# Kernel tuning notes

Measured on AMD Instinct MI355X. Metric: run time of the kernel, lower is better.

## Reference

```python
import jax, jax.numpy as jnp
import numpy as np

B, T, C, H = 2, 2048, 1024, 16
HD = C // H  # head dim = 64


def setup_inputs() -> dict:
    key = jax.random.key(0)
    ks = jax.random.split(key, 5)
    s = 0.02  # GPT-style init scale for weights
    return {
        "x": jax.random.normal(ks[0], (B, T, C), dtype=jnp.float32),
        "Wq": jax.random.normal(ks[1], (C, C), dtype=jnp.float32) * s,
        "bq": jnp.zeros((C,), dtype=jnp.float32),
        "Wk": jax.random.normal(ks[2], (C, C), dtype=jnp.float32) * s,
        "bk": jnp.zeros((C,), dtype=jnp.float32),
        "Wv": jax.random.normal(ks[3], (C, C), dtype=jnp.float32) * s,
        "bv": jnp.zeros((C,), dtype=jnp.float32),
        "Wp": jax.random.normal(ks[4], (C, C), dtype=jnp.float32) * s,
        "bp": jnp.zeros((C,), dtype=jnp.float32),
    }


def reference(x, Wq, bq, Wk, bk, Wv, bv, Wp, bp):
    b, t, c = x.shape
    # torch nn.Linear: y = x @ W.T + b  (W is [out, in])
    def heads(W, bias):
        y = jnp.einsum("btc,oc->bto", x, W) + bias
        return y.reshape(b, t, H, HD).transpose(0, 2, 1, 3)  # [B,H,T,hd]

    q = heads(Wq, bq)
    k = heads(Wk, bk)
    v = heads(Wv, bv)

    scale = 1.0 / np.sqrt(HD).astype(np.float32)
    att = jnp.einsum("bhqd,bhkd->bhqk", q, k) * scale  # [B,H,T,T]
    causal = jnp.tril(jnp.ones((t, t), dtype=bool))
    att = jnp.where(causal[None, None], att, -jnp.inf)
    att = jax.nn.softmax(att, axis=-1)
    # attn_pdrop = 0.0 -> dropout is identity
    y = jnp.einsum("bhqk,bhkd->bhqd", att, v)  # [B,H,T,hd]
    y = y.transpose(0, 2, 1, 3).reshape(b, t, c)
    y = jnp.einsum("btc,oc->bto", y, Wp) + bp  # resid_pdrop = 0.0
    return y
```

## Files before the change

### kernel.cpp

```cpp
#include <hip/hip_runtime.h>
#include <hip/hip_bf16.h>

using bf16 = __hip_bfloat16;
typedef __attribute__((ext_vector_type(8))) short short8;
typedef __attribute__((ext_vector_type(4))) float floatx4;

#define B_  2
#define T_  2048
#define C_  1024
#define H_  16
#define HD_ 64
#define BT_ (B_*T_)
#define NX_ ((size_t)BT_*C_)
#define NW_ ((size_t)C_*C_)
#define PSTR 136
#define KSCQ 0.1803368801f

__device__ __forceinline__ void gl2lds16(const bf16* g, bf16* l) {
    __builtin_amdgcn_global_load_lds((const __attribute__((address_space(1))) unsigned int*)g,
                                     (__attribute__((address_space(3))) unsigned int*)l,
                                     16, 0, 0);
}

__global__ __launch_bounds__(256) void cvt_f32_bf16(
    const float* __restrict__ x,
    const float* __restrict__ Wq, const float* __restrict__ Wk,
    const float* __restrict__ Wv, const float* __restrict__ Wp,
    bf16* __restrict__ xb, bf16* __restrict__ wqb, bf16* __restrict__ wkb,
    bf16* __restrict__ wvb, bf16* __restrict__ wpb)
{
    size_t i4 = ((size_t)blockIdx.x * 256 + threadIdx.x) * 4;
    const float* src; bf16* dst; size_t off;
    if (i4 < NX_) { src = x; dst = xb; off = i4; }
    else {
        size_t j = i4 - NX_;
        int r = (int)(j >> 20);
        off = j & (NW_ - 1);
        src = (r==0) ? Wq : (r==1) ? Wk : (r==2) ? Wv : Wp;
        dst = (r==0) ? wqb : (r==1) ? wkb : (r==2) ? wvb : wpb;
    }
    float4 v = *(const float4*)(src + off);
    union { bf16 h[4]; uint2 u; } o;
    o.h[0] = __float2bfloat16(v.x); o.h[1] = __float2bfloat16(v.y);
    o.h[2] = __float2bfloat16(v.z); o.h[3] = __float2bfloat16(v.w);
    *(uint2*)(dst + off) = o.u;
}

__global__ __launch_bounds__(256) void qkv_gemm(
    const bf16* __restrict__ x,
    const bf16* __restrict__ Wq, const float* __restrict__ bq,
    const bf16* __restrict__ Wk, const float* __restrict__ bk,
    const bf16* __restrict__ Wv, const float* __restrict__ bv,
    bf16* __restrict__ qo, bf16* __restrict__ ko, bf16* __restrict__ vt)
{
    __shared__ __align__(16) bf16 As[128*32];
    __shared__ __align__(16) bf16 Bs[128*32];

    const int tid  = threadIdx.x;
    const int w    = tid >> 6, lane = tid & 63;
    const int g    = lane >> 4, c16 = lane & 15;
    const int wr   = w >> 1,    wc  = w & 1;
    const int mtile = blockIdx.x, ntile = blockIdx.y;
    const int wsel  = ntile >> 3;
    const bf16*  W    = (wsel==0) ? Wq : (wsel==1 ? Wk : Wv);
    const float* bias = (wsel==0) ? bq : (wsel==1 ? bk : bv);
    const float oscale = (wsel==0) ? KSCQ : 1.0f;
    const int nbase  = (ntile & 7) * 128;

    const bf16* ag = x + (size_t)(mtile*128)*C_;
    const bf16* bg = W + (size_t)nbase*C_;

    floatx4 acc[4][4] = {};

    for (int k0 = 0; k0 < C_; k0 += 32) {
        #pragma unroll
        for (int p = 0; p < 2; ++p) {
            int cb = p*256 + w*64;
            int c  = cb + lane;
            gl2lds16(ag + (size_t)(c>>2)*C_ + k0 + (c&3)*8, As + cb*8);
            gl2lds16(bg + (size_t)(c>>2)*C_ + k0 + (c&3)*8, Bs + cb*8);
        }
        __syncthreads();

        short8 af[4], bfr[4];
        #pragma unroll
        for (int i = 0; i < 4; ++i)
            af[i] = *(const short8*)(As + (wr*64 + i*16 + c16)*32 + g*8);
        #pragma unroll
        for (int j = 0; j < 4; ++j)
            bfr[j] = *(const short8*)(Bs + (wc*64 + j*16 + c16)*32 + g*8);
        #pragma unroll
        for (int i = 0; i < 4; ++i)
            #pragma unroll
            for (int j = 0; j < 4; ++j)
                acc[i][j] = __builtin_amdgcn_mfma_f32_16x16x32_bf16(af[i], bfr[j], acc[i][j], 0, 0, 0);
        __syncthreads();
    }

    #pragma unroll
    for (int i = 0; i < 4; ++i) {
        int m0 = mtile*128 + wr*64 + i*16 + g*4;
        #pragma unroll
        for (int j = 0; j < 4; ++j) {
            int n = nbase + wc*64 + j*16 + c16;
            float bvf = bias[n];
            if (wsel == 2) {
                int bb = m0 >> 11, t0 = m0 & (T_-1);
                int hh = n >> 6,  hd = n & 63;
                union { bf16 hv[4]; uint2 u; } tmp;
                #pragma unroll
                for (int r = 0; r < 4; ++r) tmp.hv[r] = __float2bfloat16(acc[i][j][r] + bvf);
                *(uint2*)(vt + ((size_t)((bb*H_ + hh)*64 + hd))*T_ + t0) = tmp.u;
            } else {
                bf16* dst = (wsel==0) ? qo : ko;
                #pragma unroll
                for (int r = 0; r < 4; ++r)
                    dst[(size_t)(m0+r)*C_ + n] = __float2bfloat16((acc[i][j][r] + bvf) * oscale);
            }
        }
    }
}

__global__ __launch_bounds__(128, 2) void attn(
    const bf16* __restrict__ q, const bf16* __restrict__ k,
    const bf16* __restrict__ vt, bf16* __restrict__ y)
{
    __shared__ __align__(16) bf16    Ps[2][2][16*PSTR];
    __shared__ __align__(16) floatx4 MO[2][2][4][64];
    __shared__ __align__(16) floatx4 ML[2][2][64];
    __shared__               float   Mm[2][2][16];

    const int tid = threadIdx.x, w = tid >> 6, lane = tid & 63;
    const int g = lane >> 4, c16 = lane & 15;
    const int blk = blockIdx.x;
    const int p = blk & 31, bh = blk >> 5;
    const int h = bh & 15, b = bh >> 4;

    const bf16* kbase = k  + ((size_t)(b*T_))*C_ + h*64;
    const bf16* vbase = vt + ((size_t)(b*H_ + h))*64*T_;
    const short ONEB = 0x3F80;
    const short8 ones = {ONEB,ONEB,ONEB,ONEB,ONEB,ONEB,ONEB,ONEB};

    #pragma unroll 1
    for (int seg = 0; seg < 2; ++seg) {
        const int j  = seg ? p : 63 - p;
        const int q0 = j * 32;
        const int nit = (j >> 2) + 1;

        short8 aq[2][2];
        #pragma unroll
        for (int rt = 0; rt < 2; ++rt)
            #pragma unroll
            for (int kg = 0; kg < 2; ++kg)
                aq[rt][kg] = *(const short8*)(q + ((size_t)(b*T_ + q0 + rt*16 + c16))*C_
                                                + h*64 + kg*32 + g*8);

        floatx4 accO[2][4] = {};
        floatx4 lacc[2] = {};
        float m_l[2] = {-1e30f, -1e30f};

        #pragma unroll 1
        for (int kt = w; kt < nit; kt += 2) {
            const bf16* kp = kbase + (size_t)(kt*128 + c16)*C_ + g*8;
            short8 kb[8][2];
            #pragma unroll
            for (int ct = 0; ct < 8; ++ct)
                #pragma unroll
                for (int kg = 0; kg < 2; ++kg)
                    kb[ct][kg] = *(const short8*)(kp + (size_t)(ct*16)*C_ + kg*32);
            const bf16* vp = vbase + (size_t)c16*T_ + kt*128 + g*8;
            short8 vb[4][4];
            #pragma unroll
            for (int ks = 0; ks < 4; ++ks)
                #pragma unroll
                for (int nt = 0; nt < 4; ++nt)
                    vb[ks][nt] = *(const short8*)(vp + (size_t)(nt*16)*T_ + ks*32);

            floatx4 s[2][8];
            #pragma unroll
            for (int rt = 0; rt < 2; ++rt)
                #pragma unroll
                for (int ct = 0; ct < 8; ++ct) {
                    floatx4 a = {0.f, 0.f, 0.f, 0.f};
                    a = __builtin_amdgcn_mfma_f32_16x16x32_bf16(kb[ct][0], aq[rt][0], a, 0, 0, 0);
                    a = __builtin_amdgcn_mfma_f32_16x16x32_bf16(kb[ct][1], aq[rt][1], a, 0, 0, 0);
                    s[rt][ct] = a;
                }

            if (kt == nit-1) {
                #pragma unroll
                for (int rt = 0; rt < 2; ++rt) {
                    int qglob = q0 + rt*16 + c16;
                    #pragma unroll
                    for (int ct = 0; ct < 8; ++ct)
                        #pragma unroll
                        for (int r = 0; r < 4; ++r) {
                            int key = kt*128 + ct*16 + g*4 + r;
                            if (key > qglob) s[rt][ct][r] = -1e30f;
                        }
                }
            }

            #pragma unroll
            for (int rt = 0; rt < 2; ++rt) {
                float cm[8];
                #pragma unroll
                for (int ct = 0; ct < 8; ++ct)
                    cm[ct] = fmaxf(fmaxf(s[rt][ct][0], s[rt][ct][1]),
                                   fmaxf(s[rt][ct][2], s[rt][ct][3]));
                float tmax = fmaxf(fmaxf(fmaxf(cm[0], cm[1]), fmaxf(cm[2], cm[3])),
                                   fmaxf(fmaxf(cm[4], cm[5]), fmaxf(cm[6], cm[7])));
                tmax = fmaxf(tmax, __shfl_xor(tmax, 16));
                tmax = fmaxf(tmax, __shfl_xor(tmax, 32));
                float mn = fmaxf(m_l[rt], tmax);
                float alpha = exp2f(m_l[rt] - mn);
                m_l[rt] = mn;

                float ar[4];
                #pragma unroll
                for (int r = 0; r < 4; ++r) ar[r] = __shfl(alpha, g*4 + r);
                #pragma unroll
                for (int r = 0; r < 4; ++r) {
                    lacc[rt][r] *= ar[r];
                    #pragma unroll
                    for (int nt = 0; nt < 4; ++nt) accO[rt][nt][r] *= ar[r];
                }

                #pragma unroll
                for (int ct = 0; ct < 8; ++ct) {
                    float p0 = exp2f(s[rt][ct][0] - mn);
                    float p1 = exp2f(s[rt][ct][1] - mn);
                    float p2 = exp2f(s[rt][ct][2] - mn);
                    float p3 = exp2f(s[rt][ct][3] - mn);
                    union { __hip_bfloat162 h2[2]; uint2 u; } pk;
                    pk.h2[0] = __float22bfloat162_rn(float2{p0, p1});
                    pk.h2[1] = __float22bfloat162_rn(float2{p2, p3});
                    *(uint2*)(Ps[w][rt] + c16*PSTR + ct*16 + g*4) = pk.u;
                }
                short8 pa[4];
                #pragma unroll
                for (int ks = 0; ks < 4; ++ks)
                    pa[ks] = *(const short8*)(Ps[w][rt] + c16*PSTR + ks*32 + g*8);
                #pragma unroll
                for (int ks = 0; ks < 4; ++ks) {
                    lacc[rt] = __builtin_amdgcn_mfma_f32_16x16x32_bf16(pa[ks], ones, lacc[rt], 0, 0, 0);
                    #pragma unroll
                    for (int nt = 0; nt < 4; ++nt)
                        accO[rt][nt] = __builtin_amdgcn_mfma_f32_16x16x32_bf16(pa[ks], vb[ks][nt], accO[rt][nt], 0, 0, 0);
                }
            }
        }

        #pragma unroll
        for (int rt = 0; rt < 2; ++rt) {
            if (g == 0) Mm[w][rt][c16] = m_l[rt];
            ML[w][rt][lane] = lacc[rt];
            #pragma unroll
            for (int nt = 0; nt < 4; ++nt) MO[w][rt][nt][lane] = accO[rt][nt];
        }
        __syncthreads();

        {
            const int rt = w;
            float aA[4], aB[4];
            #pragma unroll
            for (int r = 0; r < 4; ++r) {
                float mA = Mm[0][rt][g*4 + r];
                float mB = Mm[1][rt][g*4 + r];
                float mm = fmaxf(mA, mB);
                aA[r] = exp2f(mA - mm);
                aB[r] = exp2f(mB - mm);
            }
            floatx4 lA = ML[0][rt][lane], lB = ML[1][rt][lane];
            float ir[4];
            #pragma unroll
            for (int r = 0; r < 4; ++r)
                ir[r] = __builtin_amdgcn_rcpf(lA[r]*aA[r] + lB[r]*aB[r]);
            #pragma unroll
            for (int nt = 0; nt < 4; ++nt) {
                floatx4 OA = MO[0][rt][nt][lane], OB = MO[1][rt][nt][lane];
                #pragma unroll
                for (int r = 0; r < 4; ++r) {
                    int row = q0 + rt*16 + g*4 + r;
                    float o = (OA[r]*aA[r] + OB[r]*aB[r]) * ir[r];
                    y[((size_t)(b*T_ + row))*C_ + h*64 + nt*16 + c16] = __float2bfloat16(o);
                }
            }
        }
        __syncthreads();
    }
}

__global__ __launch_bounds__(256) void proj_gemm(
    const bf16* __restrict__ yin, const bf16* __restrict__ Wp, const float* __restrict__ bp,
    float* __restrict__ out)
{
    __shared__ __align__(16) bf16 As[64*32];
    __shared__ __align__(16) bf16 Bs[128*32];

    const int tid = threadIdx.x;
    const int w = tid >> 6, lane = tid & 63;
    const int g = lane >> 4, c16 = lane & 15;
    const int wr = w >> 1, wc = w & 1;
    const int mtile = blockIdx.x, ntile = blockIdx.y;
    const int nbase = ntile * 128;

    const bf16* ag = yin + (size_t)(mtile*64)*C_;
    const bf16* bg = Wp  + (size_t)nbase*C_;

    floatx4 acc[2][4] = {};

    for (int k0 = 0; k0 < C_; k0 += 32) {
        {
            int cb = w*64;
            int c  = cb + lane;
            gl2lds16(ag + (size_t)(c>>2)*C_ + k0 + (c&3)*8, As + cb*8);
        }
        #pragma unroll
        for (int p = 0; p < 2; ++p) {
            int cb = p*256 + w*64;
            int c  = cb + lane;
            gl2lds16(bg + (size_t)(c>>2)*C_ + k0 + (c&3)*8, Bs + cb*8);
        }
        __syncthreads();

        short8 af[2], bfr[4];
        #pragma unroll
        for (int i = 0; i < 2; ++i)
            af[i] = *(const short8*)(As + (wr*32 + i*16 + c16)*32 + g*8);
        #pragma unroll
        for (int j = 0; j < 4; ++j)
            bfr[j] = *(const short8*)(Bs + (wc*64 + j*16 + c16)*32 + g*8);
        #pragma unroll
        for (int i = 0; i < 2; ++i)
            #pragma unroll
            for (int j = 0; j < 4; ++j)
                acc[i][j] = __builtin_amdgcn_mfma_f32_16x16x32_bf16(af[i], bfr[j], acc[i][j], 0, 0, 0);
        __syncthreads();
    }

    #pragma unroll
    for (int i = 0; i < 2; ++i) {
        int m0 = mtile*64 + wr*32 + i*16 + g*4;
        #pragma unroll
        for (int j = 0; j < 4; ++j) {
            int n = nbase + wc*64 + j*16 + c16;
            float bvf = bp[n];
            #pragma unroll
            for (int r = 0; r < 4; ++r)
                out[(size_t)(m0+r)*C_ + n] = acc[i][j][r] + bvf;
        }
    }
}

extern "C" void kernel_launch(void* const* d_in, const int* in_sizes, int n_in,
                              void* d_out, int out_size, void* d_ws, size_t ws_size,
                              hipStream_t stream) {
    const float* x  = (const float*)d_in[0];
    const float* Wq = (const float*)d_in[1];
    const float* bq = (const float*)d_in[2];
    const float* Wk = (const float*)d_in[3];
    const float* bk = (const float*)d_in[4];
    const float* Wv = (const float*)d_in[5];
    const float* bv = (const float*)d_in[6];
    const float* Wp = (const float*)d_in[7];
    const float* bp = (const float*)d_in[8];

    bf16* xb  = (bf16*)d_ws;
    bf16* wqb = xb  + NX_;
    bf16* wkb = wqb + NW_;
    bf16* wvb = wkb + NW_;
    bf16* wpb = wvb + NW_;
    bf16* qw  = wpb + NW_;
    bf16* kw  = qw  + NX_;
    bf16* vt  = kw  + NX_;
    bf16* yw  = vt  + NX_;

    const int cvt_blocks = (int)((NX_ + 4*NW_) / (4*256));
    cvt_f32_bf16<<<cvt_blocks, 256, 0, stream>>>(x, Wq, Wk, Wv, Wp, xb, wqb, wkb, wvb, wpb);
    qkv_gemm<<<dim3(32, 24), 256, 0, stream>>>(xb, wqb, bq, wkb, bk, wvb, bv, qw, kw, vt);
    attn    <<<1024, 128, 0, stream>>>(qw, kw, vt, yw);
    proj_gemm<<<dim3(64, 8), 256, 0, stream>>>(yw, wpb, bp, (float*)d_out);
}
```

Baseline: 217.1 us.

## Share K/V tiles in LDS across four query waves in attention

Restructures the attention kernel so each 256-thread block owns a 128-query tile. Its four waves each take 32 queries and share K and V tiles staged into LDS with global_load_lds. This replaces the old two-wave split over key tiles, which needed an LDS-based softmax merge, and cuts redundant global K/V fragment loads by sharing them across waves. In exchange it adds two block barriers per key tile with no double buffering, and load balance now depends only on reversing the tile order for the second batch instead of pairing short and long segments.

```diff
diff --git a/kernel.cpp b/kernel.cpp
--- a/kernel.cpp
+++ b/kernel.cpp
@@ -121,173 +121,146 @@
     }
 }
 
-__global__ __launch_bounds__(128, 2) void attn(
+__global__ __launch_bounds__(256, 2) void attn(
     const bf16* __restrict__ q, const bf16* __restrict__ k,
     const bf16* __restrict__ vt, bf16* __restrict__ y)
 {
-    __shared__ __align__(16) bf16    Ps[2][2][16*PSTR];
-    __shared__ __align__(16) floatx4 MO[2][2][4][64];
-    __shared__ __align__(16) floatx4 ML[2][2][64];
-    __shared__               float   Mm[2][2][16];
+    __shared__ __align__(16) bf16 Ks[16*512];
+    __shared__ __align__(16) bf16 Vs[16*512];
+    __shared__ __align__(16) bf16 Ps[4][2][16*PSTR];
 
     const int tid = threadIdx.x, w = tid >> 6, lane = tid & 63;
     const int g = lane >> 4, c16 = lane & 15;
-    const int blk = blockIdx.x;
-    const int p = blk & 31, bh = blk >> 5;
-    const int h = bh & 15, b = bh >> 4;
+    const int qraw = blockIdx.x, h = blockIdx.y, b = blockIdx.z;
+    const int qt = b ? 15 - qraw : qraw;
+    const int nit = qt + 1;
+    const int q0 = qt*128 + w*32;
 
     const bf16* kbase = k  + ((size_t)(b*T_))*C_ + h*64;
     const bf16* vbase = vt + ((size_t)(b*H_ + h))*64*T_;
     const short ONEB = 0x3F80;
     const short8 ones = {ONEB,ONEB,ONEB,ONEB,ONEB,ONEB,ONEB,ONEB};
 
+    short8 aq[2][2];
+    #pragma unroll
+    for (int rt = 0; rt < 2; ++rt)
+        #pragma unroll
+        for (int kg = 0; kg < 2; ++kg)
+            aq[rt][kg] = *(const short8*)(q + ((size_t)(b*T_ + q0 + rt*16 + c16))*C_
+                                            + h*64 + kg*32 + g*8);
+
+    floatx4 accO[2][4] = {};
+    floatx4 lacc[2] = {};
+    float m_l[2] = {-1e30f, -1e30f};
+
     #pragma unroll 1
-    for (int seg = 0; seg < 2; ++seg) {
-        const int j  = seg ? p : 63 - p;
-        const int q0 = j * 32;
-        const int nit = (j >> 2) + 1;
-
-        short8 aq[2][2];
-        #pragma unroll
-        for (int rt = 0; rt < 2; ++rt)
-            #pragma unroll
-            for (int kg = 0; kg < 2; ++kg)
-                aq[rt][kg] = *(const short8*)(q + ((size_t)(b*T_ + q0 + rt*16 + c16))*C_
-                                                + h*64 + kg*32 + g*8);
-
-        floatx4 accO[2][4] = {};
-        floatx4 lacc[2] = {};
-        float m_l[2] = {-1e30f, -1e30f};
-
-        #pragma unroll 1
-        for (int kt = w; kt < nit; kt += 2) {
-            const bf16* kp = kbase + (size_t)(kt*128 + c16)*C_ + g*8;
-            short8 kb[8][2];
+    for (int kt = 0; kt < nit; ++kt) {
+        #pragma unroll
+        for (int p = 0; p < 4; ++p) {
+            int f = w*4 + p;
+            int ctk = f >> 1, kg = f & 1;
+            gl2lds16(kbase + (size_t)(kt*128 + ctk*16 + c16)*C_ + kg*32 + g*8, Ks + f*512);
+            gl2lds16(vbase + (size_t)(p*16 + c16)*T_ + kt*128 + w*32 + g*8,    Vs + f*512);
+        }
+        __syncthreads();
+
+        floatx4 s[2][8];
+        #pragma unroll
+        for (int ct = 0; ct < 8; ++ct) {
+            short8 kb0 = *(const short8*)(Ks + (ct*2 + 0)*512 + lane*8);
+            short8 kb1 = *(const short8*)(Ks + (ct*2 + 1)*512 + lane*8);
+            #pragma unroll
+            for (int rt = 0; rt < 2; ++rt) {
+                floatx4 a = {0.f, 0.f, 0.f, 0.f};
+                a = __builtin_amdgcn_mfma_f32_16x16x32_bf16(kb0, aq[rt][0], a, 0, 0, 0);
+                a = __builtin_amdgcn_mfma_f32_16x16x32_bf16(kb1, aq[rt][1], a, 0, 0, 0);
+                s[rt][ct] = a;
+            }
+        }
+
+        if (kt == nit-1) {
+            #pragma unroll
+            for (int rt = 0; rt < 2; ++rt) {
+                int qglob = q0 + rt*16 + c16;
+                #pragma unroll
+                for (int ct = 0; ct < 8; ++ct)
+                    #pragma unroll
+                    for (int r = 0; r < 4; ++r) {
+                        int key = kt*128 + ct*16 + g*4 + r;
+                        if (key > qglob) s[rt][ct][r] = -1e30f;
+                    }
+            }
+        }
+
+        #pragma unroll
+        for (int rt = 0; rt < 2; ++rt) {
+            float cm[8];
             #pragma unroll
             for (int ct = 0; ct < 8; ++ct)
-                #pragma unroll
-                for (int kg = 0; kg < 2; ++kg)
-                    kb[ct][kg] = *(const short8*)(kp + (size_t)(ct*16)*C_ + kg*32);
-            const bf16* vp = vbase + (size_t)c16*T_ + kt*128 + g*8;
-            short8 vb[4][4];
-            #pragma unroll
-            for (int ks = 0; ks < 4; ++ks)
+                cm[ct] = fmaxf(fmaxf(s[rt][ct][0], s[rt][ct][1]),
+                               fmaxf(s[rt][ct][2], s[rt][ct][3]));
+            float tmax = fmaxf(fmaxf(fmaxf(cm[0], cm[1]), fmaxf(cm[2], cm[3])),
+                               fmaxf(fmaxf(cm[4], cm[5]), fmaxf(cm[6], cm[7])));
+            tmax = fmaxf(tmax, __shfl_xor(tmax, 16));
+            tmax = fmaxf(tmax, __shfl_xor(tmax, 32));
+            float mn = fmaxf(m_l[rt], tmax);
+            float alpha = exp2f(m_l[rt] - mn);
+            m_l[rt] = mn;
+
+            float ar[4];
+            #pragma unroll
+            for (int r = 0; r < 4; ++r) ar[r] = __shfl(alpha, g*4 + r);
+            #pragma unroll
+            for (int r = 0; r < 4; ++r) {
+                lacc[rt][r] *= ar[r];
+                #pragma unroll
+                for (int nt = 0; nt < 4; ++nt) accO[rt][nt][r] *= ar[r];
+            }
+
+            #pragma unroll
+            for (int ct = 0; ct < 8; ++ct) {
+                float p0 = exp2f(s[rt][ct][0] - mn);
+                float p1 = exp2f(s[rt][ct][1] - mn);
+                float p2 = exp2f(s[rt][ct][2] - mn);
+                float p3 = exp2f(s[rt][ct][3] - mn);
+                union { __hip_bfloat162 h2[2]; uint2 u; } pk;
+                pk.h2[0] = __float22bfloat162_rn(float2{p0, p1});
+                pk.h2[1] = __float22bfloat162_rn(float2{p2, p3});
+                *(uint2*)(Ps[w][rt] + c16*PSTR + ct*16 + g*4) = pk.u;
+            }
+        }
+
+        #pragma unroll
+        for (int ks = 0; ks < 4; ++ks) {
+            short8 vb[4];
+            #pragma unroll
+            for (int nt = 0; nt < 4; ++nt)
+                vb[nt] = *(const short8*)(Vs + (ks*4 + nt)*512 + lane*8);
+            #pragma unroll
+            for (int rt = 0; rt < 2; ++rt) {
+                short8 pa = *(const short8*)(Ps[w][rt] + c16*PSTR + ks*32 + g*8);
+                lacc[rt] = __builtin_amdgcn_mfma_f32_16x16x32_bf16(pa, ones, lacc[rt], 0, 0, 0);
                 #pragma unroll
                 for (int nt = 0; nt < 4; ++nt)
-                    vb[ks][nt] = *(const short8*)(vp + (size_t)(nt*16)*T_ + ks*32);
-
-            floatx4 s[2][8];
-            #pragma unroll
-            for (int rt = 0; rt < 2; ++rt)
-                #pragma unroll
-                for (int ct = 0; ct < 8; ++ct) {
-                    floatx4 a = {0.f, 0.f, 0.f, 0.f};
-                    a = __builtin_amdgcn_mfma_f32_16x16x32_bf16(kb[ct][0], aq[rt][0], a, 0, 0, 0);
-                    a = __builtin_amdgcn_mfma_f32_16x16x32_bf16(kb[ct][1], aq[rt][1], a, 0, 0, 0);
-                    s[rt][ct] = a;
-                }
-
-            if (kt == nit-1) {
-                #pragma unroll
-                for (int rt = 0; rt < 2; ++rt) {
-                    int qglob = q0 + rt*16 + c16;
-                    #pragma unroll
-                    for (int ct = 0; ct < 8; ++ct)
-                        #pragma unroll
-                        for (int r = 0; r < 4; ++r) {
-                            int key = kt*128 + ct*16 + g*4 + r;
-                            if (key > qglob) s[rt][ct][r] = -1e30f;
-                        }
-                }
-            }
-
-            #pragma unroll
-            for (int rt = 0; rt < 2; ++rt) {
-                float cm[8];
-                #pragma unroll
-                for (int ct = 0; ct < 8; ++ct)
-                    cm[ct] = fmaxf(fmaxf(s[rt][ct][0], s[rt][ct][1]),
-                                   fmaxf(s[rt][ct][2], s[rt][ct][3]));
-                float tmax = fmaxf(fmaxf(fmaxf(cm[0], cm[1]), fmaxf(cm[2], cm[3])),
-                                   fmaxf(fmaxf(cm[4], cm[5]), fmaxf(cm[6], cm[7])));
-                tmax = fmaxf(tmax, __shfl_xor(tmax, 16));
-                tmax = fmaxf(tmax, __shfl_xor(tmax, 32));
-                float mn = fmaxf(m_l[rt], tmax);
-                float alpha = exp2f(m_l[rt] - mn);
-                m_l[rt] = mn;
-
-                float ar[4];
-                #pragma unroll
-                for (int r = 0; r < 4; ++r) ar[r] = __shfl(alpha, g*4 + r);
-                #pragma unroll
-                for (int r = 0; r < 4; ++r) {
-                    lacc[rt][r] *= ar[r];
-                    #pragma unroll
-                    for (int nt = 0; nt < 4; ++nt) accO[rt][nt][r] *= ar[r];
-                }
-
-                #pragma unroll
-                for (int ct = 0; ct < 8; ++ct) {
-                    float p0 = exp2f(s[rt][ct][0] - mn);
-                    float p1 = exp2f(s[rt][ct][1] - mn);
-                    float p2 = exp2f(s[rt][ct][2] - mn);
-                    float p3 = exp2f(s[rt][ct][3] - mn);
-                    union { __hip_bfloat162 h2[2]; uint2 u; } pk;
-                    pk.h2[0] = __float22bfloat162_rn(float2{p0, p1});
-                    pk.h2[1] = __float22bfloat162_rn(float2{p2, p3});
-                    *(uint2*)(Ps[w][rt] + c16*PSTR + ct*16 + g*4) = pk.u;
-                }
-                short8 pa[4];
-                #pragma unroll
-                for (int ks = 0; ks < 4; ++ks)
-                    pa[ks] = *(const short8*)(Ps[w][rt] + c16*PSTR + ks*32 + g*8);
-                #pragma unroll
-                for (int ks = 0; ks < 4; ++ks) {
-                    lacc[rt] = __builtin_amdgcn_mfma_f32_16x16x32_bf16(pa[ks], ones, lacc[rt], 0, 0, 0);
-                    #pragma unroll
-                    for (int nt = 0; nt < 4; ++nt)
-                        accO[rt][nt] = __builtin_amdgcn_mfma_f32_16x16x32_bf16(pa[ks], vb[ks][nt], accO[rt][nt], 0, 0, 0);
-                }
-            }
-        }
-
-        #pragma unroll
-        for (int rt = 0; rt < 2; ++rt) {
-            if (g == 0) Mm[w][rt][c16] = m_l[rt];
-            ML[w][rt][lane] = lacc[rt];
-            #pragma unroll
-            for (int nt = 0; nt < 4; ++nt) MO[w][rt][nt][lane] = accO[rt][nt];
-        }
-        __syncthreads();
-
-        {
-            const int rt = w;
-            float aA[4], aB[4];
+                    accO[rt][nt] = __builtin_amdgcn_mfma_f32_16x16x32_bf16(pa, vb[nt], accO[rt][nt], 0, 0, 0);
+            }
+        }
+        __syncthreads();
+    }
+
+    #pragma unroll
+    for (int rt = 0; rt < 2; ++rt) {
+        float ir[4];
+        #pragma unroll
+        for (int r = 0; r < 4; ++r) ir[r] = __builtin_amdgcn_rcpf(lacc[rt][r]);
+        #pragma unroll
+        for (int nt = 0; nt < 4; ++nt)
             #pragma unroll
             for (int r = 0; r < 4; ++r) {
-                float mA = Mm[0][rt][g*4 + r];
-                float mB = Mm[1][rt][g*4 + r];
-                float mm = fmaxf(mA, mB);
-                aA[r] = exp2f(mA - mm);
-                aB[r] = exp2f(mB - mm);
-            }
-            floatx4 lA = ML[0][rt][lane], lB = ML[1][rt][lane];
-            float ir[4];
-            #pragma unroll
-            for (int r = 0; r < 4; ++r)
-                ir[r] = __builtin_amdgcn_rcpf(lA[r]*aA[r] + lB[r]*aB[r]);
-            #pragma unroll
-            for (int nt = 0; nt < 4; ++nt) {
-                floatx4 OA = MO[0][rt][nt][lane], OB = MO[1][rt][nt][lane];
-                #pragma unroll
-                for (int r = 0; r < 4; ++r) {
-                    int row = q0 + rt*16 + g*4 + r;
-                    float o = (OA[r]*aA[r] + OB[r]*aB[r]) * ir[r];
-                    y[((size_t)(b*T_ + row))*C_ + h*64 + nt*16 + c16] = __float2bfloat16(o);
-                }
-            }
-        }
-        __syncthreads();
+                int row = q0 + rt*16 + g*4 + r;
+                float o = accO[rt][nt][r] * ir[r];
+                y[((size_t)(b*T_ + row))*C_ + h*64 + nt*16 + c16] = __float2bfloat16(o);
+            }
     }
 }
 
@@ -379,6 +352,6 @@
     const int cvt_blocks = (int)((NX_ + 4*NW_) / (4*256));
     cvt_f32_bf16<<<cvt_blocks, 256, 0, stream>>>(x, Wq, Wk, Wv, Wp, xb, wqb, wkb, wvb, wpb);
     qkv_gemm<<<dim3(32, 24), 256, 0, stream>>>(xb, wqb, bq, wkb, bk, wvb, bv, qw, kw, vt);
-    attn    <<<1024, 128, 0, stream>>>(qw, kw, vt, yw);
+    attn    <<<dim3(16, H_, B_), 256, 0, stream>>>(qw, kw, vt, yw);
     proj_gemm<<<dim3(64, 8), 256, 0, stream>>>(yw, wpb, bp, (float*)d_out);
 }
```

New measurement: 210.1 us. 1.03x faster.
